# Performance work log

Measured on AMD Instinct MI355X. Metric: run time of the kernel, lower is better.

Reference implementation:

```python
import jax, jax.numpy as jnp
import numpy as np

B, T, U = 64, 256, 256
NMEL, PRE, EMB, NF, ENC, DEC, WM, VOCAB = 80, 128, 15, 128, 128, 512, 10, 44
KMAX = 5
_km = np.zeros((3, KMAX), np.float32)
for _i, _k in enumerate([1, 3, 5]):
    _km[_i, (KMAX - _k) // 2:(KMAX - _k) // 2 + _k] = 1.0
KMASK = jnp.asarray(_km)  # [3, KMAX] zero-mask embedding kernels 1/3/5 in width-5 buffers


def _lstm(x, h, c, W, b):
    z = jnp.concatenate([x, h], -1) @ W + b
    i, f, g, o = jnp.split(z, 4, -1)
    cn = jax.nn.sigmoid(f) * c + jax.nn.sigmoid(i) * jnp.tanh(g)
    hn = jax.nn.sigmoid(o) * jnp.tanh(cn)
    return hn, cn


def _conv_stack(x, w, b, residual):
    # x [B,U,Cin]; w [3,KMAX,Cin,NF]; b [3,NF]; multi-kernel-size conv1d stack
    y = 0.0
    for i in range(3):
        wk = w[i] * KMASK[i][:, None, None]
        y = y + jax.lax.conv_general_dilated(x, wk, (1,), 'SAME', dimension_numbers=('NWC', 'WIO', 'NWC')) + b[i]
    y = jax.nn.relu(y)
    return y + x if residual else y


def _forward(text, in_mels, in_mel_mask, text_mask, w_pre1, b_pre1, w_pre2, b_pre2, emb, conv_w0, conv_b0, conv_w1, conv_b1, conv_w2, conv_b2, w_bif, b_bif, w_bib, b_bib, w_attlstm, b_attlstm, w_attproj, b_attproj, w_rnn1, b_rnn1, w_rnn2, b_rnn2, w_out, b_out):
    # mel prenet (two linear layers, dropout keep-prob 1.0 -> identity)
    corr = (in_mels @ w_pre1 + b_pre1) @ w_pre2 + b_pre2  # [T,B,PRE]
    # text encoder: embedding -> conv1d stack -> BiLSTM
    x = jnp.transpose(emb[text], (1, 0, 2))  # [B,U,EMB]
    x = _conv_stack(x, conv_w0, conv_b0, False)
    x = _conv_stack(x, conv_w1, conv_b1, True)
    x = _conv_stack(x, conv_w2, conv_b2, True)
    conv_text = jnp.transpose(x, (1, 0, 2))  # [U,B,NF]
    tm = text_mask[..., None]  # [U,B,1]

    def make_bi(W, bb):
        def f(carry, xs):
            h, c = carry
            xt, mt = xs
            hn, cn = _lstm(xt, h, c, W, bb)
            hn = mt * hn + (1.0 - mt) * h
            cn = mt * cn + (1.0 - mt) * c
            return (hn, cn), hn
        return f

    z0 = (jnp.zeros((B, ENC), jnp.float32), jnp.zeros((B, ENC), jnp.float32))
    _, hf = jax.lax.scan(make_bi(w_bif, b_bif), z0, (conv_text, tm))
    _, hb = jax.lax.scan(make_bi(w_bib, b_bib), z0, (conv_text[::-1], tm[::-1]))
    ctx = jnp.concatenate([hf, hb[::-1]], -1)  # [U,B,2*ENC]

    upos = jnp.arange(U, dtype=jnp.float32)[None, :, None]  # [1,U,1]
    phi_mask = text_mask.T  # [B,U]

    def step(carry, xs):
        att_w, att_k, att_h, att_c, h1, c1, h2, c2 = carry
        corr_t, m_t = xs
        m = m_t[:, None]
        # Gaussian-mixture attention cell (Graves-style, softplus step op)
        ah, ac = _lstm(jnp.concatenate([corr_t, att_w], -1), att_h, att_c, w_attlstm, b_attlstm)
        pr = ah @ w_attproj + b_attproj  # [B,3*WM]
        a_h, b_h, k_h = jnp.split(pr, 3, -1)
        a_t = jax.nn.softplus(a_h)
        b_t = jax.nn.softplus(b_h)
        k_t = att_k + jax.nn.softplus(k_h)  # attention_scale = 1.0
        phi = (a_t[:, None, :] * jnp.exp(-b_t[:, None, :] * (k_t[:, None, :] - upos) ** 2)).sum(-1) * phi_mask  # [B,U]
        w_t = jnp.einsum('bu,ubd->bd', phi, ctx)
        w_t = m * w_t + (1.0 - m) * att_w
        k_t = m * k_t + (1.0 - m) * att_k
        ah = m * ah + (1.0 - m) * att_h
        ac = m * ac + (1.0 - m) * att_c
        h1n, c1n = _lstm(jnp.concatenate([corr_t, w_t, ah], -1), h1, c1, w_rnn1, b_rnn1)
        h1n = m * h1n + (1.0 - m) * h1
        c1n = m * c1n + (1.0 - m) * c1
        h2n, c2n = _lstm(jnp.concatenate([corr_t, w_t, h1n], -1), h2, c2, w_rnn2, b_rnn2)
        h2n = m * h2n + (1.0 - m) * h2
        c2n = m * c2n + (1.0 - m) * c2
        return (w_t, k_t, ah, ac, h1n, c1n, h2n, c2n), h2n

    zf = lambda d: jnp.zeros((B, d), jnp.float32)
    init = (zf(2 * ENC), zf(WM), zf(DEC), zf(DEC), zf(DEC), zf(DEC), zf(DEC), zf(DEC))
    _, outs = jax.lax.scan(step, init, (corr, in_mel_mask))  # outs [T,B,DEC]
    return outs @ w_out + b_out  # [T,B,NMEL]


def setup_inputs():
    key = jax.random.key(0)
    ks = iter(jax.random.split(key, 40))

    def w(shape, s=0.08):
        return jax.random.normal(next(ks), shape, jnp.float32) * s

    z = lambda *s: jnp.zeros(s, jnp.float32)
    return {
        'in_mels': jax.random.normal(next(ks), (T, B, NMEL), jnp.float32),
        'in_mel_mask': jnp.ones((T, B), jnp.float32),
        'text': jax.random.randint(next(ks), (U, B), 0, VOCAB),
        'text_mask': jnp.ones((U, B), jnp.float32),
        'w_pre1': w((NMEL, PRE)), 'b_pre1': z(PRE),
        'w_pre2': w((PRE, PRE)), 'b_pre2': z(PRE),
        'emb': w((VOCAB, EMB), 1.0),
        'conv_w0': w((3, KMAX, EMB, NF)), 'conv_b0': z(3, NF),
        'conv_w1': w((3, KMAX, NF, NF)), 'conv_b1': z(3, NF),
        'conv_w2': w((3, KMAX, NF, NF)), 'conv_b2': z(3, NF),
        'w_bif': w((NF + ENC, 4 * ENC)), 'b_bif': z(4 * ENC),
        'w_bib': w((NF + ENC, 4 * ENC)), 'b_bib': z(4 * ENC),
        'w_attlstm': w((PRE + 2 * ENC + DEC, 4 * DEC)), 'b_attlstm': z(4 * DEC),
        'w_attproj': w((DEC, 3 * WM)), 'b_attproj': z(3 * WM),
        'w_rnn1': w((PRE + 2 * ENC + 2 * DEC, 4 * DEC)), 'b_rnn1': z(4 * DEC),
        'w_rnn2': w((PRE + 2 * ENC + 2 * DEC, 4 * DEC)), 'b_rnn2': z(4 * DEC),
        'w_out': w((DEC, NMEL)), 'b_out': z(NMEL),
    }


def reference(in_mels, in_mel_mask, text, text_mask, w_pre1, b_pre1, w_pre2, b_pre2, emb, conv_w0, conv_b0, conv_w1, conv_b1, conv_w2, conv_b2, w_bif, b_bif, w_bib, b_bib, w_attlstm, b_attlstm, w_attproj, b_attproj, w_rnn1, b_rnn1, w_rnn2, b_rnn2, w_out, b_out):
    return _forward(text, in_mels, in_mel_mask, text_mask, w_pre1, b_pre1, w_pre2, b_pre2, emb, conv_w0, conv_b0, conv_w1, conv_b1, conv_w2, conv_b2, w_bif, b_bif, w_bib, b_bib, w_attlstm, b_attlstm, w_attproj, b_attproj, w_rnn1, b_rnn1, w_rnn2, b_rnn2, w_out, b_out)
```

## Files before the change

### kernel.cpp

```cpp
#include <hip/hip_runtime.h>
#include <math.h>

constexpr int NB    = 64;
constexpr int NT    = 256;
constexpr int NU    = 256;
constexpr int NMELc = 80;
constexpr int PREc  = 128;
constexpr int EMBc  = 15;
constexpr int NFc   = 128;
constexpr int ENCc  = 128;
constexpr int DECc  = 512;
constexpr int WMc   = 10;
constexpr int AKS   = 16;
constexpr size_t WSZ = (size_t)116 * 128 * 512;

using bf16x8 = __attribute__((ext_vector_type(8))) short;
using us8    = __attribute__((ext_vector_type(8))) unsigned short;
using f32x4  = __attribute__((ext_vector_type(4))) float;

__device__ __forceinline__ float sigm(float x) { return 1.0f / (1.0f + expf(-x)); }
__device__ __forceinline__ float softplusf(float x) { return fmaxf(x, 0.0f) + log1pf(expf(-fabsf(x))); }
__device__ __forceinline__ unsigned short f2bf(float f) {
  unsigned u = __builtin_bit_cast(unsigned, f);
  return (unsigned short)((u + 0x7FFFu + ((u >> 16) & 1u)) >> 16);
}
__device__ __forceinline__ float bf2f(unsigned short h) {
  return __builtin_bit_cast(float, (unsigned)h << 16);
}

template <int K, int N, int RB>
__global__ void k_dense(const float* __restrict__ X, const float* __restrict__ W,
                        const float* __restrict__ bias, float* __restrict__ Y, int R) {
  __shared__ float xs[RB][K];
  int r0 = blockIdx.x * RB;
  int tid = threadIdx.x;
  for (int idx = tid; idx < RB * K; idx += 128) {
    int r = idx / K, k = idx % K;
    xs[r][k] = (r0 + r < R) ? X[(size_t)(r0 + r) * K + k] : 0.0f;
  }
  __syncthreads();
  int j = tid;
  if (j >= N) return;
  float acc[RB];
#pragma unroll
  for (int r = 0; r < RB; ++r) acc[r] = 0.f;
  for (int k = 0; k < K; ++k) {
    float w = W[(size_t)k * N + j];
#pragma unroll
    for (int r = 0; r < RB; ++r) acc[r] += xs[r][k] * w;
  }
  float bj = bias[j];
  for (int r = 0; r < RB; ++r)
    if (r0 + r < R) Y[(size_t)(r0 + r) * N + j] = acc[r] + bj;
}

__global__ void k_embed(const int* __restrict__ text, const float* __restrict__ emb,
                        float* __restrict__ out) {
  int idx = blockIdx.x * blockDim.x + threadIdx.x;
  if (idx >= NB * NU * EMBc) return;
  int c = idx % EMBc;
  int bu = idx / EMBc;
  int u = bu % NU, b = bu / NU;
  out[idx] = emb[text[u * NB + b] * EMBc + c];
}

template <int CIN>
__global__ void k_weff(const float* __restrict__ w, const float* __restrict__ bb,
                       float* __restrict__ weff, float* __restrict__ beff) {
  int idx = blockIdx.x * blockDim.x + threadIdx.x;
  const int tot = 5 * CIN * NFc;
  if (idx < tot) {
    int f = idx % NFc;
    int tc = idx / NFc;
    int c = tc % CIN, t = tc / CIN;
    float m0 = (t == 2) ? 1.f : 0.f;
    float m1 = (t >= 1 && t <= 3) ? 1.f : 0.f;
    float w0 = w[((size_t)(0 * 5 + t) * CIN + c) * NFc + f];
    float w1 = w[((size_t)(1 * 5 + t) * CIN + c) * NFc + f];
    float w2 = w[((size_t)(2 * 5 + t) * CIN + c) * NFc + f];
    weff[idx] = w0 * m0 + w1 * m1 + w2;
  }
  if (idx < NFc) beff[idx] = bb[idx] + bb[NFc + idx] + bb[2 * NFc + idx];
}

template <int CIN, bool RES>
__global__ void k_conv(const float* __restrict__ x, const float* __restrict__ weff,
                       const float* __restrict__ beff, float* __restrict__ y) {
  const int UT = 8;
  __shared__ float xs[(UT + 4) * CIN];
  int b = blockIdx.y, u0 = blockIdx.x * UT;
  int tid = threadIdx.x;
  for (int idx = tid; idx < (UT + 4) * CIN; idx += 128) {
    int c = idx % CIN;
    int uu = idx / CIN;
    int u = u0 + uu - 2;
    xs[idx] = (u >= 0 && u < NU) ? x[((size_t)b * NU + u) * CIN + c] : 0.f;
  }
  __syncthreads();
  int f = tid;
  float acc[UT];
#pragma unroll
  for (int r = 0; r < UT; ++r) acc[r] = beff[f];
  for (int t = 0; t < 5; ++t)
    for (int c = 0; c < CIN; ++c) {
      float w = weff[((size_t)t * CIN + c) * NFc + f];
#pragma unroll
      for (int r = 0; r < UT; ++r) acc[r] += xs[(r + t) * CIN + c] * w;
    }
  for (int r = 0; r < UT; ++r) {
    float v = fmaxf(acc[r], 0.f);
    if (RES) v += xs[(r + 2) * CIN + f];
    y[((size_t)b * NU + u0 + r) * NFc + f] = v;
  }
}

__global__ __launch_bounds__(128) void k_enc2(int u, int gate_only,
                                              const float* __restrict__ Wf, const float* __restrict__ bf,
                                              const float* __restrict__ Wb, const float* __restrict__ bb_,
                                              const float* __restrict__ convt,
                                              const float* __restrict__ text_mask,
                                              float* __restrict__ ctx, float* __restrict__ hbuf,
                                              float* __restrict__ cbuf, float* __restrict__ zE) {
  const size_t ZPS = (size_t)8 * NB * 512;
  __shared__ float hs[4][128];
  __shared__ float xs[4][64];
  int tid = threadIdx.x;
  int g = blockIdx.x, q = blockIdx.y, d = blockIdx.z;
  int b0 = g * 4;
  const float* Wd = d ? Wb : Wf;
  const float* bd = d ? bb_ : bf;
  int j = tid;
  if (u > 0) {
    int ig = u - 1;
    int upos = d ? (NU - 1 - ig) : ig;
    const float* zr = zE + (size_t)((u - 1) & 1) * ZPS + (size_t)d * 4 * NB * 512;
    for (int bi = 0; bi < 4; ++bi) {
      int b = b0 + bi;
      float zi = bd[j], zf = bd[128 + j], zg = bd[256 + j], zo = bd[384 + j];
      for (int qq = 0; qq < 4; ++qq) {
        const float* p = zr + ((size_t)qq * NB + b) * 512;
        zi += p[j];
        zf += p[128 + j];
        zg += p[256 + j];
        zo += p[384 + j];
      }
      float cp = 0.f, hp = 0.f;
      if (u >= 2) {
        cp = cbuf[((size_t)(d * 2 + (u & 1)) * NB + b) * 128 + j];
        hp = hbuf[((size_t)(d * 2 + (u & 1)) * NB + b) * 128 + j];
      }
      float cn = sigm(zf) * cp + sigm(zi) * tanhf(zg);
      float hn = sigm(zo) * tanhf(cn);
      float mt = text_mask[upos * NB + b];
      hn = mt * hn + (1.f - mt) * hp;
      cn = mt * cn + (1.f - mt) * cp;
      hs[bi][j] = hn;
      if (q == 0) {
        hbuf[((size_t)(d * 2 + ((u - 1) & 1)) * NB + b) * 128 + j] = hn;
        cbuf[((size_t)(d * 2 + ((u - 1) & 1)) * NB + b) * 128 + j] = cn;
        ctx[((size_t)upos * NB + b) * 256 + d * 128 + j] = hn;
      }
    }
  } else {
#pragma unroll
    for (int bi = 0; bi < 4; ++bi) hs[bi][j] = 0.f;
  }
  if (gate_only) return;
  __syncthreads();
  int k0 = q * 64;
  {
    int upos_x = d ? (NU - 1 - u) : u;
    for (int idx = tid; idx < 4 * 64; idx += 128) {
      int bi = idx >> 6, kk = idx & 63;
      int k = k0 + kk;
      float v = (k < 128) ? convt[((size_t)(b0 + bi) * NU + upos_x) * 128 + k] : hs[bi][k - 128];
      xs[bi][kk] = v;
    }
  }
  __syncthreads();
  float4 acc[4];
#pragma unroll
  for (int bi = 0; bi < 4; ++bi) acc[bi] = make_float4(0.f, 0.f, 0.f, 0.f);
  const float4* Wp = (const float4*)Wd + (size_t)k0 * 128 + tid;
#pragma unroll 8
  for (int kk = 0; kk < 64; ++kk) {
    float4 w = Wp[(size_t)kk * 128];
#pragma unroll
    for (int bi = 0; bi < 4; ++bi) {
      float xv = xs[bi][kk];
      acc[bi].x += w.x * xv;
      acc[bi].y += w.y * xv;
      acc[bi].z += w.z * xv;
      acc[bi].w += w.w * xv;
    }
  }
  float4* zw = (float4*)(zE + (size_t)(u & 1) * ZPS) + ((size_t)(d * 4 + q) * NB + b0) * 128 + tid;
#pragma unroll
  for (int bi = 0; bi < 4; ++bi) zw[(size_t)bi * 128] = acc[bi];
}

__global__ __launch_bounds__(256) void k_wcvt(const float* __restrict__ w1,
                                              const float* __restrict__ wa,
                                              const float* __restrict__ w2,
                                              unsigned short* __restrict__ Wpk) {
  int ktg = blockIdx.x;
  int ntg = blockIdx.y;
  const float* W;
  int ktl;
  if (ktg < 44) { W = w1; ktl = ktg; }
  else if (ktg < 72) { W = wa; ktl = ktg - 44; }
  else { W = w2; ktl = ktg - 72; }
  int tid = threadIdx.x;
  for (int p = 0; p < 8; ++p) {
    int idx = p * 256 + tid;
    int ntl = idx >> 6, l = idx & 63;
    int nt = ntg * 32 + ntl;
    us8 vh, vl;
#pragma unroll
    for (int j = 0; j < 8; ++j) {
      float wv = W[(size_t)(ktl * 32 + (l >> 4) * 8 + j) * 2048 + nt * 16 + (l & 15)];
      unsigned short h = f2bf(wv);
      vh[j] = h;
      vl[j] = f2bf(wv - bf2f(h));
    }
    size_t o = (((size_t)ktg * 128 + nt) * 64 + l) * 8;
    *(us8*)(Wpk + o) = vh;
    *(us8*)(Wpk + WSZ + o) = vl;
  }
}

struct DecAp {
  const float* corr;
  const unsigned short* Wpk;
  const float *aw, *ah, *h1, *outs, *zerob;
  float* zX;
};
__global__ __launch_bounds__(256) void k_decA(DecAp P, int i) {
  __shared__ unsigned short xsh[16][360];
  __shared__ unsigned short xsl[16][360];
  int tid = threadIdx.x, bid = blockIdx.x;
  int bg = bid / 96, r = bid % 96, c = r >> 3, nc = r & 7;
  int g, ktg0, nkt, k0;
  if (c < 4)      { g = 0; ktg0 = c * 11;            nkt = 11; k0 = c * 352; }
  else if (c < 8) { g = 1; ktg0 = 44 + (c - 4) * 7;  nkt = 7;  k0 = (c - 4) * 224; }
  else            { g = 2; ktg0 = 72 + (c - 8) * 11; nkt = 11; k0 = (c - 8) * 352; }
  int s = (g == 0) ? (i - 1) : (g == 1 ? i : (i - 2));
  if (s < 0 || s >= NT) return;

  const float* p0 = P.corr + (size_t)s * NB * PREc;
  const float *p1, *p2, *p3;
  int s1, s2_, s3;
  if (g == 1) {
    bool z = (s == 0);
    int pp = (s - 1) & 1;
    p1 = z ? P.zerob : P.aw + (size_t)pp * NB * 256; s1 = z ? 0 : 256;
    p2 = z ? P.zerob : P.ah + (size_t)pp * NB * DECc; s2_ = z ? 0 : DECc;
    p3 = P.zerob; s3 = 0;
  } else if (g == 0) {
    int pp = s & 1;
    p1 = P.aw + (size_t)pp * NB * 256; s1 = 256;
    p2 = P.ah + (size_t)pp * NB * DECc; s2_ = DECc;
    bool z = (s == 0);
    p3 = z ? P.zerob : P.h1 + (size_t)((s - 1) & 1) * NB * DECc; s3 = z ? 0 : DECc;
  } else {
    int pp = s & 1;
    p1 = P.aw + (size_t)pp * NB * 256; s1 = 256;
    p2 = P.h1 + (size_t)pp * NB * DECc; s2_ = DECc;
    bool z = (s == 0);
    p3 = z ? P.zerob : P.outs + (size_t)(s - 1) * NB * DECc; s3 = z ? 0 : DECc;
  }
  int klen = nkt * 32;
  for (int idx = tid; idx < klen; idx += 256) {
    int k = k0 + idx;
#pragma unroll 4
    for (int bi = 0; bi < 16; ++bi) {
      int b = bg * 16 + bi;
      float v;
      int kx = k;
      if (kx < PREc)
        v = p0[(size_t)b * PREc + kx];
      else {
        kx -= PREc;
        if (kx < 256)
          v = p1[(size_t)b * s1 + kx];
        else {
          kx -= 256;
          if (kx < DECc)
            v = p2[(size_t)b * s2_ + kx];
          else
            v = p3[(size_t)b * s3 + (kx - DECc)];
        }
      }
      unsigned short h = f2bf(v);
      xsh[bi][idx] = h;
      xsl[bi][idx] = f2bf(v - bf2f(h));
    }
  }
  __syncthreads();
  int w = tid >> 6, lane = tid & 63;
  const unsigned short* wbh =
      P.Wpk + ((size_t)ktg0 * 128 + (size_t)(nc * 16 + w * 4)) * 512 + lane * 8;
  const unsigned short* wbl = wbh + WSZ;
  const unsigned short* xh = &xsh[lane & 15][(lane >> 4) * 8];
  const unsigned short* xl = &xsl[lane & 15][(lane >> 4) * 8];
  f32x4 acc0 = {0.f, 0.f, 0.f, 0.f}, acc1 = acc0, acc2 = acc0, acc3 = acc0;
  for (int kt = 0; kt < nkt; ++kt) {
    bf16x8 a_h = *(const bf16x8*)(xh + kt * 32);
    bf16x8 a_l = *(const bf16x8*)(xl + kt * 32);
    const unsigned short* wph = wbh + (size_t)kt * 65536;
    const unsigned short* wpl = wbl + (size_t)kt * 65536;
    bf16x8 b0h = *(const bf16x8*)(wph);
    bf16x8 b1h = *(const bf16x8*)(wph + 512);
    bf16x8 b2h = *(const bf16x8*)(wph + 1024);
    bf16x8 b3h = *(const bf16x8*)(wph + 1536);
    bf16x8 b0l = *(const bf16x8*)(wpl);
    bf16x8 b1l = *(const bf16x8*)(wpl + 512);
    bf16x8 b2l = *(const bf16x8*)(wpl + 1024);
    bf16x8 b3l = *(const bf16x8*)(wpl + 1536);
    acc0 = __builtin_amdgcn_mfma_f32_16x16x32_bf16(a_h, b0h, acc0, 0, 0, 0);
    acc1 = __builtin_amdgcn_mfma_f32_16x16x32_bf16(a_h, b1h, acc1, 0, 0, 0);
    acc2 = __builtin_amdgcn_mfma_f32_16x16x32_bf16(a_h, b2h, acc2, 0, 0, 0);
    acc3 = __builtin_amdgcn_mfma_f32_16x16x32_bf16(a_h, b3h, acc3, 0, 0, 0);
    acc0 = __builtin_amdgcn_mfma_f32_16x16x32_bf16(a_l, b0h, acc0, 0, 0, 0);
    acc1 = __builtin_amdgcn_mfma_f32_16x16x32_bf16(a_l, b1h, acc1, 0, 0, 0);
    acc2 = __builtin_amdgcn_mfma_f32_16x16x32_bf16(a_l, b2h, acc2, 0, 0, 0);
    acc3 = __builtin_amdgcn_mfma_f32_16x16x32_bf16(a_l, b3h, acc3, 0, 0, 0);
    acc0 = __builtin_amdgcn_mfma_f32_16x16x32_bf16(a_h, b0l, acc0, 0, 0, 0);
    acc1 = __builtin_amdgcn_mfma_f32_16x16x32_bf16(a_h, b1l, acc1, 0, 0, 0);
    acc2 = __builtin_amdgcn_mfma_f32_16x16x32_bf16(a_h, b2l, acc2, 0, 0, 0);
    acc3 = __builtin_amdgcn_mfma_f32_16x16x32_bf16(a_h, b3l, acc3, 0, 0, 0);
  }
  int brow = bg * 16 + (lane >> 4) * 4;
  float* zb = P.zX + ((size_t)c * NB + brow) * 2048 + nc * 256 + w * 64 + (lane & 15);
#pragma unroll
  for (int rr = 0; rr < 4; ++rr) zb[(size_t)rr * 2048 + 0] = acc0[rr];
#pragma unroll
  for (int rr = 0; rr < 4; ++rr) zb[(size_t)rr * 2048 + 16] = acc1[rr];
#pragma unroll
  for (int rr = 0; rr < 4; ++rr) zb[(size_t)rr * 2048 + 32] = acc2[rr];
#pragma unroll
  for (int rr = 0; rr < 4; ++rr) zb[(size_t)rr * 2048 + 48] = acc3[rr];
}

struct DecBp {
  const float *mel_mask, *text_mask, *ctx, *zX;
  const float *b_att, *b_rnn1, *b_rnn2, *w_proj, *b_proj;
  float *aw, *ak, *ah, *ac, *h1, *c1, *c2, *outs;
};

__device__ __forceinline__ void do_gate(const float* zX, int clo, int chi, const float* bias,
                                        const float* cprev, const float* hprev, bool zfirst,
                                        const float* mm, float* hout, float* cout, int b, int j) {
  float2 zi = *(const float2*)(bias + j);
  float2 zf = *(const float2*)(bias + 512 + j);
  float2 zg = *(const float2*)(bias + 1024 + j);
  float2 zo = *(const float2*)(bias + 1536 + j);
  for (int c = clo; c <= chi; ++c) {
    const float* q = zX + ((size_t)c * NB + b) * 2048 + j;
    float2 a = *(const float2*)q;
    float2 f2 = *(const float2*)(q + 512);
    float2 g2 = *(const float2*)(q + 1024);
    float2 o2 = *(const float2*)(q + 1536);
    zi.x += a.x; zi.y += a.y;
    zf.x += f2.x; zf.y += f2.y;
    zg.x += g2.x; zg.y += g2.y;
    zo.x += o2.x; zo.y += o2.y;
  }
  float2 cp = zfirst ? make_float2(0.f, 0.f) : *(const float2*)(cprev + (size_t)b * 512 + j);
  float2 hp = zfirst ? make_float2(0.f, 0.f) : *(const float2*)(hprev + (size_t)b * 512 + j);
  float m = mm[b];
  float cnx = sigm(zf.x) * cp.x + sigm(zi.x) * tanhf(zg.x);
  float cny = sigm(zf.y) * cp.y + sigm(zi.y) * tanhf(zg.y);
  float hnx = sigm(zo.x) * tanhf(cnx);
  float hny = sigm(zo.y) * tanhf(cny);
  *(float2*)(hout + (size_t)b * 512 + j) =
      make_float2(m * hnx + (1.f - m) * hp.x, m * hny + (1.f - m) * hp.y);
  *(float2*)(cout + (size_t)b * 512 + j) =
      make_float2(m * cnx + (1.f - m) * cp.x, m * cny + (1.f - m) * cp.y);
}

__global__ __launch_bounds__(256) void k_decB(DecBp P, int i) {
  __shared__ float sh[1152];
  int tid = threadIdx.x, bid = blockIdx.x;
  if (bid < 64) {
    int s = i - 1;
    if (s < 0 || s >= NT) return;
    bool z = (s == 0);
    do_gate(P.zX, 0, 3, P.b_rnn1,
            z ? P.zX : P.c1 + (size_t)((s - 1) & 1) * NB * 512,
            z ? P.zX : P.h1 + (size_t)((s - 1) & 1) * NB * 512, z,
            P.mel_mask + (size_t)s * NB,
            P.h1 + (size_t)(s & 1) * NB * 512,
            P.c1 + (size_t)(s & 1) * NB * 512, bid, 2 * tid);
    return;
  }
  if (bid < 128) {
    int s = i - 2;
    if (s < 0 || s >= NT) return;
    bool z = (s == 0);
    do_gate(P.zX, 8, 11, P.b_rnn2,
            z ? P.zX : P.c2 + (size_t)((s - 1) & 1) * NB * 512,
            z ? P.zX : P.outs + (size_t)(s - 1) * NB * 512, z,
            P.mel_mask + (size_t)s * NB,
            P.outs + (size_t)s * NB * 512,
            P.c2 + (size_t)(s & 1) * NB * 512, bid - 64, 2 * tid);
    return;
  }
  int s = i;
  if (s >= NT) return;
  int b = bid - 128;
  float* ah_s = sh;
  float* red_s = sh + 512;
  float* pr_s = sh + 768;
  float* abk = sh + 800;
  float* phi_s = sh + 896;
  float m = P.mel_mask[(size_t)s * NB + b];
  bool z = (s == 0);
  int pp = (s - 1) & 1;
  {
    int j = 2 * tid;
    float2 zi = *(const float2*)(P.b_att + j);
    float2 zf = *(const float2*)(P.b_att + 512 + j);
    float2 zg = *(const float2*)(P.b_att + 1024 + j);
    float2 zo = *(const float2*)(P.b_att + 1536 + j);
    for (int cc = 4; cc <= 7; ++cc) {
      const float* q = P.zX + ((size_t)cc * NB + b) * 2048 + j;
      float2 a = *(const float2*)q;
      float2 f2 = *(const float2*)(q + 512);
      float2 g2 = *(const float2*)(q + 1024);
      float2 o2 = *(const float2*)(q + 1536);
      zi.x += a.x; zi.y += a.y;
      zf.x += f2.x; zf.y += f2.y;
      zg.x += g2.x; zg.y += g2.y;
      zo.x += o2.x; zo.y += o2.y;
    }
    float2 cp = z ? make_float2(0.f, 0.f)
                  : *(const float2*)(P.ac + (size_t)pp * NB * 512 + (size_t)b * 512 + j);
    float2 hp = z ? make_float2(0.f, 0.f)
                  : *(const float2*)(P.ah + (size_t)pp * NB * 512 + (size_t)b * 512 + j);
    float cnx = sigm(zf.x) * cp.x + sigm(zi.x) * tanhf(zg.x);
    float cny = sigm(zf.y) * cp.y + sigm(zi.y) * tanhf(zg.y);
    float hrx = sigm(zo.x) * tanhf(cnx);
    float hry = sigm(zo.y) * tanhf(cny);
    ah_s[j] = hrx;
    ah_s[j + 1] = hry;
    *(float2*)(P.ah + (size_t)(s & 1) * NB * 512 + (size_t)b * 512 + j) =
        make_float2(m * hrx + (1.f - m) * hp.x, m * hry + (1.f - m) * hp.y);
    *(float2*)(P.ac + (size_t)(s & 1) * NB * 512 + (size_t)b * 512 + j) =
        make_float2(m * cnx + (1.f - m) * cp.x, m * cny + (1.f - m) * cp.y);
  }
  __syncthreads();
  {
    int cc2 = tid & 31, ch = tid >> 5;
    float ssum = 0.f;
    if (cc2 < 30)
      for (int k = ch * 64; k < ch * 64 + 64; ++k) ssum += ah_s[k] * P.w_proj[k * 30 + cc2];
    red_s[ch * 32 + cc2] = ssum;
  }
  __syncthreads();
  if (tid < 30) {
    float ssum = P.b_proj[tid];
    for (int ch = 0; ch < 8; ++ch) ssum += red_s[ch * 32 + tid];
    pr_s[tid] = ssum;
  }
  __syncthreads();
  if (tid < WMc) {
    float kp = z ? 0.f : P.ak[(size_t)pp * NB * AKS + (size_t)b * AKS + tid];
    float a_t = softplusf(pr_s[tid]);
    float b_t = softplusf(pr_s[WMc + tid]);
    float k_t = kp + softplusf(pr_s[2 * WMc + tid]);
    abk[tid] = a_t;
    abk[32 + tid] = b_t;
    abk[64 + tid] = k_t;
    P.ak[(size_t)(s & 1) * NB * AKS + (size_t)b * AKS + tid] = m * k_t + (1.f - m) * kp;
  }
  __syncthreads();
  {
    int u = tid;
    float ssum = 0.f;
#pragma unroll
    for (int gg = 0; gg < WMc; ++gg) {
      float dd = abk[64 + gg] - (float)u;
      ssum += abk[gg] * expf(-abk[32 + gg] * dd * dd);
    }
    phi_s[u] = ssum * P.text_mask[u * NB + b];
  }
  __syncthreads();
  {
    int dcol = tid;
    float ssum = 0.f;
#pragma unroll 8
    for (int u = 0; u < NU; ++u)
      ssum += phi_s[u] * __builtin_nontemporal_load(P.ctx + ((size_t)u * NB + b) * 256 + dcol);
    float wprev = z ? 0.f : P.aw[(size_t)pp * NB * 256 + (size_t)b * 256 + dcol];
    P.aw[(size_t)(s & 1) * NB * 256 + (size_t)b * 256 + dcol] = m * ssum + (1.f - m) * wprev;
  }
}

extern "C" void kernel_launch(void* const* d_in, const int* in_sizes, int n_in,
                              void* d_out, int out_size, void* d_ws, size_t ws_size,
                              hipStream_t stream) {
  const float* in_mels = (const float*)d_in[0];
  const float* mel_mask = (const float*)d_in[1];
  const int* text = (const int*)d_in[2];
  const float* text_mask = (const float*)d_in[3];
  const float* w_pre1 = (const float*)d_in[4];
  const float* b_pre1 = (const float*)d_in[5];
  const float* w_pre2 = (const float*)d_in[6];
  const float* b_pre2 = (const float*)d_in[7];
  const float* emb = (const float*)d_in[8];
  const float* conv_w0 = (const float*)d_in[9];
  const float* conv_b0 = (const float*)d_in[10];
  const float* conv_w1 = (const float*)d_in[11];
  const float* conv_b1 = (const float*)d_in[12];
  const float* conv_w2 = (const float*)d_in[13];
  const float* conv_b2 = (const float*)d_in[14];
  const float* w_bif = (const float*)d_in[15];
  const float* b_bif = (const float*)d_in[16];
  const float* w_bib = (const float*)d_in[17];
  const float* b_bib = (const float*)d_in[18];
  const float* w_att = (const float*)d_in[19];
  const float* b_att = (const float*)d_in[20];
  const float* w_proj = (const float*)d_in[21];
  const float* b_proj = (const float*)d_in[22];
  const float* w_rnn1 = (const float*)d_in[23];
  const float* b_rnn1 = (const float*)d_in[24];
  const float* w_rnn2 = (const float*)d_in[25];
  const float* b_rnn2 = (const float*)d_in[26];
  const float* w_outp = (const float*)d_in[27];
  const float* b_outp = (const float*)d_in[28];

  float* ws = (float*)d_ws;
  size_t off = 0;
  auto alloc = [&](size_t n) {
    float* p = ws + off;
    off += (n + 63) & ~(size_t)63;
    return p;
  };
  float* corr = alloc((size_t)NT * NB * PREc);
  float* embx = alloc((size_t)NB * NU * EMBc);
  float* wpkR = alloc(WSZ);
  float* zX = alloc((size_t)12 * NB * 2048);
  float* ctx = alloc((size_t)NU * NB * 2 * ENCc);
  float* zE = alloc((size_t)2 * 8 * NB * 512);
  float* hbufE = alloc((size_t)4 * NB * ENCc);
  float* cbufE = alloc((size_t)4 * NB * ENCc);
  float* aw = alloc((size_t)2 * NB * 2 * ENCc);
  float* ak = alloc((size_t)2 * NB * AKS);
  float* ah = alloc((size_t)2 * NB * DECc);
  float* ac = alloc((size_t)2 * NB * DECc);
  float* h1 = alloc((size_t)2 * NB * DECc);
  float* c1 = alloc((size_t)2 * NB * DECc);
  float* c2 = alloc((size_t)2 * NB * DECc);
  float* outs = alloc((size_t)NT * NB * DECc);
  float* weff0 = alloc((size_t)5 * EMBc * NFc);
  float* beff0 = alloc(NFc);
  float* weff1 = alloc((size_t)5 * NFc * NFc);
  float* beff1 = alloc(NFc);
  float* weff2 = alloc((size_t)5 * NFc * NFc);
  float* beff2 = alloc(NFc);
  float* zerob = alloc(1024);

  unsigned short* Wpk = (unsigned short*)wpkR;
  float* tmp = wpkR;
  float* convA = wpkR;
  float* convB = ctx;
  float* convOut = outs;

  hipMemsetAsync(zerob, 0, 1024 * sizeof(float), stream);

  k_dense<NMELc, PREc, 8><<<NT * NB / 8, 128, 0, stream>>>(in_mels, w_pre1, b_pre1, tmp, NT * NB);
  k_dense<PREc, PREc, 8><<<NT * NB / 8, 128, 0, stream>>>(tmp, w_pre2, b_pre2, corr, NT * NB);

  k_embed<<<(NB * NU * EMBc + 255) / 256, 256, 0, stream>>>(text, emb, embx);
  k_weff<EMBc><<<(5 * EMBc * NFc + 255) / 256, 256, 0, stream>>>(conv_w0, conv_b0, weff0, beff0);
  k_weff<NFc><<<(5 * NFc * NFc + 255) / 256, 256, 0, stream>>>(conv_w1, conv_b1, weff1, beff1);
  k_weff<NFc><<<(5 * NFc * NFc + 255) / 256, 256, 0, stream>>>(conv_w2, conv_b2, weff2, beff2);
  k_conv<EMBc, false><<<dim3(NU / 8, NB), 128, 0, stream>>>(embx, weff0, beff0, convB);
  k_conv<NFc, true><<<dim3(NU / 8, NB), 128, 0, stream>>>(convB, weff1, beff1, convA);
  k_conv<NFc, true><<<dim3(NU / 8, NB), 128, 0, stream>>>(convA, weff2, beff2, convOut);

  k_wcvt<<<dim3(116, 4), 256, 0, stream>>>(w_rnn1, w_att, w_rnn2, Wpk);

  for (int u = 0; u <= NU; ++u) {
    dim3 g(NB / 4, (u == NU) ? 1 : 4, 2);
    k_enc2<<<g, 128, 0, stream>>>(u, (u == NU) ? 1 : 0, w_bif, b_bif, w_bib, b_bib, convOut,
                                  text_mask, ctx, hbufE, cbufE, zE);
  }

  DecAp A;
  A.corr = corr; A.Wpk = Wpk;
  A.aw = aw; A.ah = ah; A.h1 = h1; A.outs = outs; A.zerob = zerob;
  A.zX = zX;
  DecBp Bp;
  Bp.mel_mask = mel_mask; Bp.text_mask = text_mask; Bp.ctx = ctx; Bp.zX = zX;
  Bp.b_att = b_att; Bp.b_rnn1 = b_rnn1; Bp.b_rnn2 = b_rnn2;
  Bp.w_proj = w_proj; Bp.b_proj = b_proj;
  Bp.aw = aw; Bp.ak = ak; Bp.ah = ah; Bp.ac = ac;
  Bp.h1 = h1; Bp.c1 = c1; Bp.c2 = c2; Bp.outs = outs;
  for (int i = 0; i <= NT + 1; ++i) {
    k_decA<<<384, 256, 0, stream>>>(A, i);
    k_decB<<<192, 256, 0, stream>>>(Bp, i);
  }

  k_dense<DECc, NMELc, 8><<<NT * NB / 8, 128, 0, stream>>>(outs, w_outp, b_outp, (float*)d_out,
                                                           NT * NB);
}
```

Baseline: 13.25 ms.

## Hoist encoder input GEMM, run BiLSTM persistently, fuse decoder kernels with flags

```diff
diff --git a/kernel.cpp b/kernel.cpp
--- a/kernel.cpp
+++ b/kernel.cpp
@@ -26,6 +26,23 @@
 }
 __device__ __forceinline__ float bf2f(unsigned short h) {
   return __builtin_bit_cast(float, (unsigned)h << 16);
+}
+__device__ __forceinline__ float ldF(const float* p) {
+  return __hip_atomic_load(p, __ATOMIC_RELAXED, __HIP_MEMORY_SCOPE_AGENT);
+}
+__device__ __forceinline__ void stF(float* p, float v) {
+  __hip_atomic_store(p, v, __ATOMIC_RELAXED, __HIP_MEMORY_SCOPE_AGENT);
+}
+__device__ __forceinline__ float2 ldF2(const float* p) {
+  unsigned long long u = __hip_atomic_load((const unsigned long long*)p, __ATOMIC_RELAXED,
+                                           __HIP_MEMORY_SCOPE_AGENT);
+  return __builtin_bit_cast(float2, u);
+}
+__device__ __forceinline__ unsigned ldU(const unsigned* p) {
+  return __hip_atomic_load(p, __ATOMIC_RELAXED, __HIP_MEMORY_SCOPE_AGENT);
+}
+__device__ __forceinline__ void stU(unsigned* p, unsigned v) {
+  __hip_atomic_store(p, v, __ATOMIC_RELAXED, __HIP_MEMORY_SCOPE_AGENT);
 }
 
 template <int K, int N, int RB>
@@ -114,89 +131,106 @@
   }
 }
 
-__global__ __launch_bounds__(128) void k_enc2(int u, int gate_only,
-                                              const float* __restrict__ Wf, const float* __restrict__ bf,
-                                              const float* __restrict__ Wb, const float* __restrict__ bb_,
-                                              const float* __restrict__ convt,
-                                              const float* __restrict__ text_mask,
-                                              float* __restrict__ ctx, float* __restrict__ hbuf,
-                                              float* __restrict__ cbuf, float* __restrict__ zE) {
-  const size_t ZPS = (size_t)8 * NB * 512;
-  __shared__ float hs[4][128];
-  __shared__ float xs[4][64];
-  int tid = threadIdx.x;
-  int g = blockIdx.x, q = blockIdx.y, d = blockIdx.z;
-  int b0 = g * 4;
+__global__ __launch_bounds__(512) void k_zx(const float* __restrict__ Wf,
+                                            const float* __restrict__ bf,
+                                            const float* __restrict__ Wb,
+                                            const float* __restrict__ bb_,
+                                            const float* __restrict__ convt,
+                                            _Float16* __restrict__ zx) {
+  __shared__ float xs[8][128];
+  int du = blockIdx.x;
+  int d = du >> 8, u = du & 255;
+  int bg = blockIdx.y;
   const float* Wd = d ? Wb : Wf;
   const float* bd = d ? bb_ : bf;
+  int upos_x = d ? (NU - 1 - u) : u;
+  int tid = threadIdx.x;
+  for (int idx = tid; idx < 8 * 128; idx += 512) {
+    int bi = idx >> 7, k = idx & 127;
+    xs[bi][k] = convt[((size_t)(bg * 8 + bi) * NU + upos_x) * 128 + k];
+  }
+  __syncthreads();
   int j = tid;
-  if (u > 0) {
-    int ig = u - 1;
-    int upos = d ? (NU - 1 - ig) : ig;
-    const float* zr = zE + (size_t)((u - 1) & 1) * ZPS + (size_t)d * 4 * NB * 512;
-    for (int bi = 0; bi < 4; ++bi) {
+  float acc[8];
+#pragma unroll
+  for (int r = 0; r < 8; ++r) acc[r] = 0.f;
+  for (int k = 0; k < 128; ++k) {
+    float w = Wd[(size_t)k * 512 + j];
+#pragma unroll
+    for (int r = 0; r < 8; ++r) acc[r] += xs[r][k] * w;
+  }
+  float bj = bd[j];
+#pragma unroll
+  for (int r = 0; r < 8; ++r)
+    zx[(((size_t)d * 256 + u) * 64 + bg * 8 + r) * 512 + j] = (_Float16)(acc[r] + bj);
+}
+
+__global__ __launch_bounds__(256) void k_encP2(const float* __restrict__ Wf,
+                                               const float* __restrict__ Wb,
+                                               const _Float16* __restrict__ zx,
+                                               const float* __restrict__ text_mask,
+                                               float* __restrict__ ctx) {
+  __shared__ float hs[4][128];
+  __shared__ float zs[4][512];
+  int bid = blockIdx.x;
+  int d = bid & 1, g = bid >> 1;
+  int b0 = g * 4;
+  const float* Wh = (d ? Wb : Wf) + (size_t)128 * 512;
+  int tid = threadIdx.x;
+  int q = tid >> 6, lane = tid & 63;
+  int col0 = q * 128 + 2 * lane;
+  float creg[2] = {0.f, 0.f};
+  for (int idx = tid; idx < 512; idx += 256) hs[idx >> 7][idx & 127] = 0.f;
+  __syncthreads();
+  for (int u = 0; u < NU; ++u) {
+    const _Float16* zxu = zx + (((size_t)d * 256 + u) * 64 + b0) * 512;
+#pragma unroll
+    for (int p = 0; p < 8; ++p) {
+      int idx = p * 256 + tid;
+      int bi = idx >> 9, cc = idx & 511;
+      zs[bi][cc] = (float)zxu[(size_t)bi * 512 + cc];
+    }
+    __syncthreads();
+    if (u > 0) {
+      float2 acc[4];
+#pragma unroll
+      for (int bi = 0; bi < 4; ++bi) acc[bi] = make_float2(0.f, 0.f);
+#pragma unroll 4
+      for (int kk = 0; kk < 128; ++kk) {
+        float2 w = *(const float2*)&Wh[(size_t)kk * 512 + col0];
+#pragma unroll
+        for (int bi = 0; bi < 4; ++bi) {
+          float h = hs[bi][kk];
+          acc[bi].x += w.x * h;
+          acc[bi].y += w.y * h;
+        }
+      }
+#pragma unroll
+      for (int bi = 0; bi < 4; ++bi) {
+        zs[bi][col0] += acc[bi].x;
+        zs[bi][col0 + 1] += acc[bi].y;
+      }
+      __syncthreads();
+    }
+    int upos = d ? (NU - 1 - u) : u;
+#pragma unroll
+    for (int e = 0; e < 2; ++e) {
+      int idx = 2 * tid + e;
+      int bi = idx >> 7, j = idx & 127;
       int b = b0 + bi;
-      float zi = bd[j], zf = bd[128 + j], zg = bd[256 + j], zo = bd[384 + j];
-      for (int qq = 0; qq < 4; ++qq) {
-        const float* p = zr + ((size_t)qq * NB + b) * 512;
-        zi += p[j];
-        zf += p[128 + j];
-        zg += p[256 + j];
-        zo += p[384 + j];
-      }
-      float cp = 0.f, hp = 0.f;
-      if (u >= 2) {
-        cp = cbuf[((size_t)(d * 2 + (u & 1)) * NB + b) * 128 + j];
-        hp = hbuf[((size_t)(d * 2 + (u & 1)) * NB + b) * 128 + j];
-      }
+      float zi = zs[bi][j], zf = zs[bi][128 + j], zg = zs[bi][256 + j], zo = zs[bi][384 + j];
+      float cp = creg[e], hp = hs[bi][j];
       float cn = sigm(zf) * cp + sigm(zi) * tanhf(zg);
       float hn = sigm(zo) * tanhf(cn);
       float mt = text_mask[upos * NB + b];
       hn = mt * hn + (1.f - mt) * hp;
       cn = mt * cn + (1.f - mt) * cp;
+      creg[e] = cn;
       hs[bi][j] = hn;
-      if (q == 0) {
-        hbuf[((size_t)(d * 2 + ((u - 1) & 1)) * NB + b) * 128 + j] = hn;
-        cbuf[((size_t)(d * 2 + ((u - 1) & 1)) * NB + b) * 128 + j] = cn;
-        ctx[((size_t)upos * NB + b) * 256 + d * 128 + j] = hn;
-      }
-    }
-  } else {
-#pragma unroll
-    for (int bi = 0; bi < 4; ++bi) hs[bi][j] = 0.f;
-  }
-  if (gate_only) return;
-  __syncthreads();
-  int k0 = q * 64;
-  {
-    int upos_x = d ? (NU - 1 - u) : u;
-    for (int idx = tid; idx < 4 * 64; idx += 128) {
-      int bi = idx >> 6, kk = idx & 63;
-      int k = k0 + kk;
-      float v = (k < 128) ? convt[((size_t)(b0 + bi) * NU + upos_x) * 128 + k] : hs[bi][k - 128];
-      xs[bi][kk] = v;
-    }
-  }
-  __syncthreads();
-  float4 acc[4];
-#pragma unroll
-  for (int bi = 0; bi < 4; ++bi) acc[bi] = make_float4(0.f, 0.f, 0.f, 0.f);
-  const float4* Wp = (const float4*)Wd + (size_t)k0 * 128 + tid;
-#pragma unroll 8
-  for (int kk = 0; kk < 64; ++kk) {
-    float4 w = Wp[(size_t)kk * 128];
-#pragma unroll
-    for (int bi = 0; bi < 4; ++bi) {
-      float xv = xs[bi][kk];
-      acc[bi].x += w.x * xv;
-      acc[bi].y += w.y * xv;
-      acc[bi].z += w.z * xv;
-      acc[bi].w += w.w * xv;
-    }
-  }
-  float4* zw = (float4*)(zE + (size_t)(u & 1) * ZPS) + ((size_t)(d * 4 + q) * NB + b0) * 128 + tid;
-#pragma unroll
-  for (int bi = 0; bi < 4; ++bi) zw[(size_t)bi * 128] = acc[bi];
+      ctx[((size_t)upos * NB + b) * 256 + d * 128 + j] = hn;
+    }
+    __syncthreads();
+  }
 }
 
 __global__ __launch_bounds__(256) void k_wcvt(const float* __restrict__ w1,
@@ -229,138 +263,39 @@
   }
 }
 
-struct DecAp {
+struct DecMp {
   const float* corr;
   const unsigned short* Wpk;
-  const float *aw, *ah, *h1, *outs, *zerob;
+  const float *mel_mask, *text_mask, *ctx;
+  const float *b_att, *b_rnn1, *b_rnn2, *w_proj, *b_proj;
+  float *aw, *ak, *ah, *ac, *h1, *c1, *c2, *outs, *zerob;
   float* zX;
+  unsigned* flags;
 };
-__global__ __launch_bounds__(256) void k_decA(DecAp P, int i) {
-  __shared__ unsigned short xsh[16][360];
-  __shared__ unsigned short xsl[16][360];
-  int tid = threadIdx.x, bid = blockIdx.x;
-  int bg = bid / 96, r = bid % 96, c = r >> 3, nc = r & 7;
-  int g, ktg0, nkt, k0;
-  if (c < 4)      { g = 0; ktg0 = c * 11;            nkt = 11; k0 = c * 352; }
-  else if (c < 8) { g = 1; ktg0 = 44 + (c - 4) * 7;  nkt = 7;  k0 = (c - 4) * 224; }
-  else            { g = 2; ktg0 = 72 + (c - 8) * 11; nkt = 11; k0 = (c - 8) * 352; }
-  int s = (g == 0) ? (i - 1) : (g == 1 ? i : (i - 2));
-  if (s < 0 || s >= NT) return;
-
-  const float* p0 = P.corr + (size_t)s * NB * PREc;
-  const float *p1, *p2, *p3;
-  int s1, s2_, s3;
-  if (g == 1) {
-    bool z = (s == 0);
-    int pp = (s - 1) & 1;
-    p1 = z ? P.zerob : P.aw + (size_t)pp * NB * 256; s1 = z ? 0 : 256;
-    p2 = z ? P.zerob : P.ah + (size_t)pp * NB * DECc; s2_ = z ? 0 : DECc;
-    p3 = P.zerob; s3 = 0;
-  } else if (g == 0) {
-    int pp = s & 1;
-    p1 = P.aw + (size_t)pp * NB * 256; s1 = 256;
-    p2 = P.ah + (size_t)pp * NB * DECc; s2_ = DECc;
-    bool z = (s == 0);
-    p3 = z ? P.zerob : P.h1 + (size_t)((s - 1) & 1) * NB * DECc; s3 = z ? 0 : DECc;
-  } else {
-    int pp = s & 1;
-    p1 = P.aw + (size_t)pp * NB * 256; s1 = 256;
-    p2 = P.h1 + (size_t)pp * NB * DECc; s2_ = DECc;
-    bool z = (s == 0);
-    p3 = z ? P.zerob : P.outs + (size_t)(s - 1) * NB * DECc; s3 = z ? 0 : DECc;
-  }
-  int klen = nkt * 32;
-  for (int idx = tid; idx < klen; idx += 256) {
-    int k = k0 + idx;
-#pragma unroll 4
-    for (int bi = 0; bi < 16; ++bi) {
-      int b = bg * 16 + bi;
-      float v;
-      int kx = k;
-      if (kx < PREc)
-        v = p0[(size_t)b * PREc + kx];
-      else {
-        kx -= PREc;
-        if (kx < 256)
-          v = p1[(size_t)b * s1 + kx];
-        else {
-          kx -= 256;
-          if (kx < DECc)
-            v = p2[(size_t)b * s2_ + kx];
-          else
-            v = p3[(size_t)b * s3 + (kx - DECc)];
-        }
-      }
-      unsigned short h = f2bf(v);
-      xsh[bi][idx] = h;
-      xsl[bi][idx] = f2bf(v - bf2f(h));
-    }
-  }
-  __syncthreads();
-  int w = tid >> 6, lane = tid & 63;
-  const unsigned short* wbh =
-      P.Wpk + ((size_t)ktg0 * 128 + (size_t)(nc * 16 + w * 4)) * 512 + lane * 8;
-  const unsigned short* wbl = wbh + WSZ;
-  const unsigned short* xh = &xsh[lane & 15][(lane >> 4) * 8];
-  const unsigned short* xl = &xsl[lane & 15][(lane >> 4) * 8];
-  f32x4 acc0 = {0.f, 0.f, 0.f, 0.f}, acc1 = acc0, acc2 = acc0, acc3 = acc0;
-  for (int kt = 0; kt < nkt; ++kt) {
-    bf16x8 a_h = *(const bf16x8*)(xh + kt * 32);
-    bf16x8 a_l = *(const bf16x8*)(xl + kt * 32);
-    const unsigned short* wph = wbh + (size_t)kt * 65536;
-    const unsigned short* wpl = wbl + (size_t)kt * 65536;
-    bf16x8 b0h = *(const bf16x8*)(wph);
-    bf16x8 b1h = *(const bf16x8*)(wph + 512);
-    bf16x8 b2h = *(const bf16x8*)(wph + 1024);
-    bf16x8 b3h = *(const bf16x8*)(wph + 1536);
-    bf16x8 b0l = *(const bf16x8*)(wpl);
-    bf16x8 b1l = *(const bf16x8*)(wpl + 512);
-    bf16x8 b2l = *(const bf16x8*)(wpl + 1024);
-    bf16x8 b3l = *(const bf16x8*)(wpl + 1536);
-    acc0 = __builtin_amdgcn_mfma_f32_16x16x32_bf16(a_h, b0h, acc0, 0, 0, 0);
-    acc1 = __builtin_amdgcn_mfma_f32_16x16x32_bf16(a_h, b1h, acc1, 0, 0, 0);
-    acc2 = __builtin_amdgcn_mfma_f32_16x16x32_bf16(a_h, b2h, acc2, 0, 0, 0);
-    acc3 = __builtin_amdgcn_mfma_f32_16x16x32_bf16(a_h, b3h, acc3, 0, 0, 0);
-    acc0 = __builtin_amdgcn_mfma_f32_16x16x32_bf16(a_l, b0h, acc0, 0, 0, 0);
-    acc1 = __builtin_amdgcn_mfma_f32_16x16x32_bf16(a_l, b1h, acc1, 0, 0, 0);
-    acc2 = __builtin_amdgcn_mfma_f32_16x16x32_bf16(a_l, b2h, acc2, 0, 0, 0);
-    acc3 = __builtin_amdgcn_mfma_f32_16x16x32_bf16(a_l, b3h, acc3, 0, 0, 0);
-    acc0 = __builtin_amdgcn_mfma_f32_16x16x32_bf16(a_h, b0l, acc0, 0, 0, 0);
-    acc1 = __builtin_amdgcn_mfma_f32_16x16x32_bf16(a_h, b1l, acc1, 0, 0, 0);
-    acc2 = __builtin_amdgcn_mfma_f32_16x16x32_bf16(a_h, b2l, acc2, 0, 0, 0);
-    acc3 = __builtin_amdgcn_mfma_f32_16x16x32_bf16(a_h, b3l, acc3, 0, 0, 0);
-  }
-  int brow = bg * 16 + (lane >> 4) * 4;
-  float* zb = P.zX + ((size_t)c * NB + brow) * 2048 + nc * 256 + w * 64 + (lane & 15);
-#pragma unroll
-  for (int rr = 0; rr < 4; ++rr) zb[(size_t)rr * 2048 + 0] = acc0[rr];
-#pragma unroll
-  for (int rr = 0; rr < 4; ++rr) zb[(size_t)rr * 2048 + 16] = acc1[rr];
-#pragma unroll
-  for (int rr = 0; rr < 4; ++rr) zb[(size_t)rr * 2048 + 32] = acc2[rr];
-#pragma unroll
-  for (int rr = 0; rr < 4; ++rr) zb[(size_t)rr * 2048 + 48] = acc3[rr];
-}
-
-struct DecBp {
-  const float *mel_mask, *text_mask, *ctx, *zX;
-  const float *b_att, *b_rnn1, *b_rnn2, *w_proj, *b_proj;
-  float *aw, *ak, *ah, *ac, *h1, *c1, *c2, *outs;
-};
-
-__device__ __forceinline__ void do_gate(const float* zX, int clo, int chi, const float* bias,
-                                        const float* cprev, const float* hprev, bool zfirst,
-                                        const float* mm, float* hout, float* cout, int b, int j) {
+
+__device__ __forceinline__ void wait_flags(const unsigned* flags, int base, unsigned target) {
+  int tid = threadIdx.x;
+  for (;;) {
+    bool ok = true;
+    if (tid < 128) {
+      int f = (tid < 64) ? (base + tid) : (192 + base + (tid - 64));
+      ok = (ldU(&flags[f]) >= target);
+    }
+    if (__syncthreads_and(ok)) break;
+    __builtin_amdgcn_s_sleep(8);
+  }
+}
+
+__device__ __forceinline__ void do_gateM(const float* zX, int clo, int chi, const float* bias,
+                                         const float* cprev, const float* hprev, bool zfirst,
+                                         const float* mm, float* hout, float* cout, int b, int j) {
   float2 zi = *(const float2*)(bias + j);
   float2 zf = *(const float2*)(bias + 512 + j);
   float2 zg = *(const float2*)(bias + 1024 + j);
   float2 zo = *(const float2*)(bias + 1536 + j);
   for (int c = clo; c <= chi; ++c) {
     const float* q = zX + ((size_t)c * NB + b) * 2048 + j;
-    float2 a = *(const float2*)q;
-    float2 f2 = *(const float2*)(q + 512);
-    float2 g2 = *(const float2*)(q + 1024);
-    float2 o2 = *(const float2*)(q + 1536);
+    float2 a = ldF2(q), f2 = ldF2(q + 512), g2 = ldF2(q + 1024), o2 = ldF2(q + 1536);
     zi.x += a.x; zi.y += a.y;
     zf.x += f2.x; zf.y += f2.y;
     zg.x += g2.x; zg.y += g2.y;
@@ -379,36 +314,148 @@
       make_float2(m * cnx + (1.f - m) * cp.x, m * cny + (1.f - m) * cp.y);
 }
 
-__global__ __launch_bounds__(256) void k_decB(DecBp P, int i) {
-  __shared__ float sh[1152];
+__global__ __launch_bounds__(256) void k_decM(DecMp P, int i) {
+  __shared__ __align__(16) unsigned short xsh[32][360];
+  __shared__ __align__(16) unsigned short xsl[32][360];
   int tid = threadIdx.x, bid = blockIdx.x;
-  if (bid < 64) {
+  if (bid < 384) {
+    int bg = bid / 192, r = bid % 192, c = r >> 4, nc = r & 15;
+    int g, ktg0, nkt, k0;
+    if (c < 4)      { g = 0; ktg0 = c * 11;            nkt = 11; k0 = c * 352; }
+    else if (c < 8) { g = 1; ktg0 = 44 + (c - 4) * 7;  nkt = 7;  k0 = (c - 4) * 224; }
+    else            { g = 2; ktg0 = 72 + (c - 8) * 11; nkt = 11; k0 = (c - 8) * 352; }
+    int s = (g == 0) ? (i - 1) : (g == 1 ? i : (i - 2));
+    if (s >= 0 && s < NT) {
+      const float* p0 = P.corr + (size_t)s * NB * PREc;
+      const float *p1, *p2, *p3;
+      int s1, s2_, s3;
+      if (g == 1) {
+        bool z = (s == 0);
+        int pp = (s - 1) & 1;
+        p1 = z ? P.zerob : P.aw + (size_t)pp * NB * 256; s1 = z ? 0 : 256;
+        p2 = z ? P.zerob : P.ah + (size_t)pp * NB * DECc; s2_ = z ? 0 : DECc;
+        p3 = P.zerob; s3 = 0;
+      } else if (g == 0) {
+        int pp = s & 1;
+        p1 = P.aw + (size_t)pp * NB * 256; s1 = 256;
+        p2 = P.ah + (size_t)pp * NB * DECc; s2_ = DECc;
+        bool z = (s == 0);
+        p3 = z ? P.zerob : P.h1 + (size_t)((s - 1) & 1) * NB * DECc; s3 = z ? 0 : DECc;
+      } else {
+        int pp = s & 1;
+        p1 = P.aw + (size_t)pp * NB * 256; s1 = 256;
+        p2 = P.h1 + (size_t)pp * NB * DECc; s2_ = DECc;
+        bool z = (s == 0);
+        p3 = z ? P.zerob : P.outs + (size_t)(s - 1) * NB * DECc; s3 = z ? 0 : DECc;
+      }
+      int klen = nkt * 32;
+      for (int idx = tid; idx < klen; idx += 256) {
+        int k = k0 + idx;
+#pragma unroll 4
+        for (int bi = 0; bi < 32; ++bi) {
+          int b = bg * 32 + bi;
+          float v;
+          int kx = k;
+          if (kx < PREc)
+            v = p0[(size_t)b * PREc + kx];
+          else {
+            kx -= PREc;
+            if (kx < 256)
+              v = p1[(size_t)b * s1 + kx];
+            else {
+              kx -= 256;
+              if (kx < DECc)
+                v = p2[(size_t)b * s2_ + kx];
+              else
+                v = p3[(size_t)b * s3 + (kx - DECc)];
+            }
+          }
+          unsigned short h = f2bf(v);
+          xsh[bi][idx] = h;
+          xsl[bi][idx] = f2bf(v - bf2f(h));
+        }
+      }
+      __syncthreads();
+      int w = tid >> 6, lane = tid & 63;
+      const unsigned short* wb0 =
+          P.Wpk + (((size_t)ktg0 * 128 + (size_t)(nc * 8 + w * 2)) * 64 + lane) * 8;
+      f32x4 acc[2][2];
+#pragma unroll
+      for (int m = 0; m < 2; ++m)
+#pragma unroll
+        for (int t = 0; t < 2; ++t) acc[m][t] = f32x4{0.f, 0.f, 0.f, 0.f};
+      int arow0 = lane & 15, acol = (lane >> 4) * 8;
+      for (int kt = 0; kt < nkt; ++kt) {
+        bf16x8 ah0 = *(const bf16x8*)&xsh[arow0][kt * 32 + acol];
+        bf16x8 ah1 = *(const bf16x8*)&xsh[16 + arow0][kt * 32 + acol];
+        bf16x8 al0 = *(const bf16x8*)&xsl[arow0][kt * 32 + acol];
+        bf16x8 al1 = *(const bf16x8*)&xsl[16 + arow0][kt * 32 + acol];
+        const unsigned short* wp = wb0 + (size_t)kt * 65536;
+        bf16x8 b0h = *(const bf16x8*)(wp);
+        bf16x8 b1h = *(const bf16x8*)(wp + 512);
+        bf16x8 b0l = *(const bf16x8*)(wp + WSZ);
+        bf16x8 b1l = *(const bf16x8*)(wp + WSZ + 512);
+        acc[0][0] = __builtin_amdgcn_mfma_f32_16x16x32_bf16(ah0, b0h, acc[0][0], 0, 0, 0);
+        acc[0][1] = __builtin_amdgcn_mfma_f32_16x16x32_bf16(ah0, b1h, acc[0][1], 0, 0, 0);
+        acc[1][0] = __builtin_amdgcn_mfma_f32_16x16x32_bf16(ah1, b0h, acc[1][0], 0, 0, 0);
+        acc[1][1] = __builtin_amdgcn_mfma_f32_16x16x32_bf16(ah1, b1h, acc[1][1], 0, 0, 0);
+        acc[0][0] = __builtin_amdgcn_mfma_f32_16x16x32_bf16(al0, b0h, acc[0][0], 0, 0, 0);
+        acc[0][1] = __builtin_amdgcn_mfma_f32_16x16x32_bf16(al0, b1h, acc[0][1], 0, 0, 0);
+        acc[1][0] = __builtin_amdgcn_mfma_f32_16x16x32_bf16(al1, b0h, acc[1][0], 0, 0, 0);
+        acc[1][1] = __builtin_amdgcn_mfma_f32_16x16x32_bf16(al1, b1h, acc[1][1], 0, 0, 0);
+        acc[0][0] = __builtin_amdgcn_mfma_f32_16x16x32_bf16(ah0, b0l, acc[0][0], 0, 0, 0);
+        acc[0][1] = __builtin_amdgcn_mfma_f32_16x16x32_bf16(ah0, b1l, acc[0][1], 0, 0, 0);
+        acc[1][0] = __builtin_amdgcn_mfma_f32_16x16x32_bf16(ah1, b0l, acc[1][0], 0, 0, 0);
+        acc[1][1] = __builtin_amdgcn_mfma_f32_16x16x32_bf16(ah1, b1l, acc[1][1], 0, 0, 0);
+      }
+#pragma unroll
+      for (int m = 0; m < 2; ++m)
+#pragma unroll
+        for (int t = 0; t < 2; ++t) {
+          int brow = bg * 32 + m * 16 + (lane >> 4) * 4;
+          int col = nc * 128 + (w * 2 + t) * 16 + (lane & 15);
+          float* zb = P.zX + ((size_t)c * NB + brow) * 2048 + col;
+#pragma unroll
+          for (int rr = 0; rr < 4; ++rr) stF(zb + (size_t)rr * 2048, acc[m][t][rr]);
+        }
+    }
+    __syncthreads();
+    if (tid == 0) stU(&P.flags[bid], (unsigned)(i + 1));
+    return;
+  }
+  int wb = bid - 384;
+  unsigned target = (unsigned)(i + 1);
+  if (wb < 64) {
     int s = i - 1;
     if (s < 0 || s >= NT) return;
+    wait_flags(P.flags, 0, target);
     bool z = (s == 0);
-    do_gate(P.zX, 0, 3, P.b_rnn1,
-            z ? P.zX : P.c1 + (size_t)((s - 1) & 1) * NB * 512,
-            z ? P.zX : P.h1 + (size_t)((s - 1) & 1) * NB * 512, z,
-            P.mel_mask + (size_t)s * NB,
-            P.h1 + (size_t)(s & 1) * NB * 512,
-            P.c1 + (size_t)(s & 1) * NB * 512, bid, 2 * tid);
+    do_gateM(P.zX, 0, 3, P.b_rnn1,
+             z ? P.zerob : P.c1 + (size_t)((s - 1) & 1) * NB * 512,
+             z ? P.zerob : P.h1 + (size_t)((s - 1) & 1) * NB * 512, z,
+             P.mel_mask + (size_t)s * NB,
+             P.h1 + (size_t)(s & 1) * NB * 512,
+             P.c1 + (size_t)(s & 1) * NB * 512, wb, 2 * tid);
     return;
   }
-  if (bid < 128) {
+  if (wb < 128) {
     int s = i - 2;
     if (s < 0 || s >= NT) return;
+    wait_flags(P.flags, 128, target);
     bool z = (s == 0);
-    do_gate(P.zX, 8, 11, P.b_rnn2,
-            z ? P.zX : P.c2 + (size_t)((s - 1) & 1) * NB * 512,
-            z ? P.zX : P.outs + (size_t)(s - 1) * NB * 512, z,
-            P.mel_mask + (size_t)s * NB,
-            P.outs + (size_t)s * NB * 512,
-            P.c2 + (size_t)(s & 1) * NB * 512, bid - 64, 2 * tid);
+    do_gateM(P.zX, 8, 11, P.b_rnn2,
+             z ? P.zerob : P.c2 + (size_t)((s - 1) & 1) * NB * 512,
+             z ? P.zerob : P.outs + (size_t)(s - 1) * NB * 512, z,
+             P.mel_mask + (size_t)s * NB,
+             P.outs + (size_t)s * NB * 512,
+             P.c2 + (size_t)(s & 1) * NB * 512, wb - 64, 2 * tid);
     return;
   }
   int s = i;
   if (s >= NT) return;
-  int b = bid - 128;
+  wait_flags(P.flags, 64, target);
+  int b = wb - 128;
+  float* sh = (float*)&xsh[0][0];
   float* ah_s = sh;
   float* red_s = sh + 512;
   float* pr_s = sh + 768;
@@ -425,10 +472,7 @@
     float2 zo = *(const float2*)(P.b_att + 1536 + j);
     for (int cc = 4; cc <= 7; ++cc) {
       const float* q = P.zX + ((size_t)cc * NB + b) * 2048 + j;
-      float2 a = *(const float2*)q;
-      float2 f2 = *(const float2*)(q + 512);
-      float2 g2 = *(const float2*)(q + 1024);
-      float2 o2 = *(const float2*)(q + 1536);
+      float2 a = ldF2(q), f2 = ldF2(q + 512), g2 = ldF2(q + 1024), o2 = ldF2(q + 1536);
       zi.x += a.x; zi.y += a.y;
       zf.x += f2.x; zf.y += f2.y;
       zg.x += g2.x; zg.y += g2.y;
@@ -542,9 +586,7 @@
   float* wpkR = alloc(WSZ);
   float* zX = alloc((size_t)12 * NB * 2048);
   float* ctx = alloc((size_t)NU * NB * 2 * ENCc);
-  float* zE = alloc((size_t)2 * 8 * NB * 512);
-  float* hbufE = alloc((size_t)4 * NB * ENCc);
-  float* cbufE = alloc((size_t)4 * NB * ENCc);
+  float* convbuf = alloc((size_t)NB * NU * NFc);
   float* aw = alloc((size_t)2 * NB * 2 * ENCc);
   float* ak = alloc((size_t)2 * NB * AKS);
   float* ah = alloc((size_t)2 * NB * DECc);
@@ -560,14 +602,17 @@
   float* weff2 = alloc((size_t)5 * NFc * NFc);
   float* beff2 = alloc(NFc);
   float* zerob = alloc(1024);
+  float* flagsf = alloc(512);
+  unsigned* flags = (unsigned*)flagsf;
 
   unsigned short* Wpk = (unsigned short*)wpkR;
+  _Float16* zx = (_Float16*)outs;
   float* tmp = wpkR;
   float* convA = wpkR;
   float* convB = ctx;
-  float* convOut = outs;
 
   hipMemsetAsync(zerob, 0, 1024 * sizeof(float), stream);
+  hipMemsetAsync(flags, 0, 512 * sizeof(unsigned), stream);
 
   k_dense<NMELc, PREc, 8><<<NT * NB / 8, 128, 0, stream>>>(in_mels, w_pre1, b_pre1, tmp, NT * NB);
   k_dense<PREc, PREc, 8><<<NT * NB / 8, 128, 0, stream>>>(tmp, w_pre2, b_pre2, corr, NT * NB);
@@ -578,29 +623,23 @@
   k_weff<NFc><<<(5 * NFc * NFc + 255) / 256, 256, 0, stream>>>(conv_w2, conv_b2, weff2, beff2);
   k_conv<EMBc, false><<<dim3(NU / 8, NB), 128, 0, stream>>>(embx, weff0, beff0, convB);
   k_conv<NFc, true><<<dim3(NU / 8, NB), 128, 0, stream>>>(convB, weff1, beff1, convA);
-  k_conv<NFc, true><<<dim3(NU / 8, NB), 128, 0, stream>>>(convA, weff2, beff2, convOut);
+  k_conv<NFc, true><<<dim3(NU / 8, NB), 128, 0, stream>>>(convA, weff2, beff2, convbuf);
 
   k_wcvt<<<dim3(116, 4), 256, 0, stream>>>(w_rnn1, w_att, w_rnn2, Wpk);
 
-  for (int u = 0; u <= NU; ++u) {
-    dim3 g(NB / 4, (u == NU) ? 1 : 4, 2);
-    k_enc2<<<g, 128, 0, stream>>>(u, (u == NU) ? 1 : 0, w_bif, b_bif, w_bib, b_bib, convOut,
-                                  text_mask, ctx, hbufE, cbufE, zE);
-  }
-
-  DecAp A;
-  A.corr = corr; A.Wpk = Wpk;
-  A.aw = aw; A.ah = ah; A.h1 = h1; A.outs = outs; A.zerob = zerob;
-  A.zX = zX;
-  DecBp Bp;
-  Bp.mel_mask = mel_mask; Bp.text_mask = text_mask; Bp.ctx = ctx; Bp.zX = zX;
-  Bp.b_att = b_att; Bp.b_rnn1 = b_rnn1; Bp.b_rnn2 = b_rnn2;
-  Bp.w_proj = w_proj; Bp.b_proj = b_proj;
-  Bp.aw = aw; Bp.ak = ak; Bp.ah = ah; Bp.ac = ac;
-  Bp.h1 = h1; Bp.c1 = c1; Bp.c2 = c2; Bp.outs = outs;
+  k_zx<<<dim3(512, 8), 512, 0, stream>>>(w_bif, b_bif, w_bib, b_bib, convbuf, zx);
+  k_encP2<<<32, 256, 0, stream>>>(w_bif, w_bib, zx, text_mask, ctx);
+
+  DecMp M;
+  M.corr = corr; M.Wpk = Wpk;
+  M.mel_mask = mel_mask; M.text_mask = text_mask; M.ctx = ctx;
+  M.b_att = b_att; M.b_rnn1 = b_rnn1; M.b_rnn2 = b_rnn2;
+  M.w_proj = w_proj; M.b_proj = b_proj;
+  M.aw = aw; M.ak = ak; M.ah = ah; M.ac = ac;
+  M.h1 = h1; M.c1 = c1; M.c2 = c2; M.outs = outs; M.zerob = zerob;
+  M.zX = zX; M.flags = flags;
   for (int i = 0; i <= NT + 1; ++i) {
-    k_decA<<<384, 256, 0, stream>>>(A, i);
-    k_decB<<<192, 256, 0, stream>>>(Bp, i);
+    k_decM<<<576, 256, 0, stream>>>(M, i);
   }
 
   k_dense<DECc, NMELc, 8><<<NT * NB / 8, 128, 0, stream>>>(outs, w_outp, b_outp, (float*)d_out,
```

Result: no change. 13.05 ms (-1.5%).
